# Optimization experiments

Hardware: AMD Instinct MI355X
Metric: run time of the kernel (lower is better)

The kernel has to match this reference:

```python
import jax, jax.numpy as jnp
import numpy as np

N, E, B = 10000, 160000, 64
ND, ED, H, L, C = 128, 64, 256, 4, 10
LN_EPS = 1e-5


def _layernorm(x, g, b):
    mu = jnp.mean(x, axis=-1, keepdims=True)
    var = jnp.mean(jnp.square(x - mu), axis=-1, keepdims=True)
    return (x - mu) * jax.lax.rsqrt(var + LN_EPS) * g + b


def setup_inputs() -> dict:
    key = jax.random.key(0)
    ks = jax.random.split(key, 24)

    def w(k, shape, fan_in):
        return jax.random.normal(k, shape, jnp.float32) * (1.0 / np.sqrt(fan_in))

    node_features = jax.random.normal(ks[0], (N, ND), jnp.float32)
    edge_index = jax.random.randint(ks[1], (2, E), 0, N, jnp.int64)
    edge_features = jax.random.normal(ks[2], (E, ED), jnp.float32)
    # deterministic sorted batch assignment (no empty graphs)
    batch = (jnp.arange(N, dtype=jnp.int64) * B) // N

    inp = dict(
        node_features=node_features,
        edge_index=edge_index,
        edge_features=edge_features,
        batch=batch,
        node_W=w(ks[3], (ND, H), ND), node_b=jnp.zeros((H,), jnp.float32),
        edge_W=w(ks[4], (ED, H), ED), edge_b=jnp.zeros((H,), jnp.float32),
        msg_W1=w(ks[5], (L, 3 * H, H), 3 * H), msg_b1=jnp.zeros((L, H), jnp.float32),
        msg_W2=w(ks[6], (L, H, H), H), msg_b2=jnp.zeros((L, H), jnp.float32),
        upd_W1=w(ks[7], (L, 2 * H, H), 2 * H), upd_b1=jnp.zeros((L, H), jnp.float32),
        upd_W2=w(ks[8], (L, H, H), H), upd_b2=jnp.zeros((L, H), jnp.float32),
        ln_g=jnp.ones((L, H), jnp.float32), ln_b=jnp.zeros((L, H), jnp.float32),
        ro_W1=w(ks[9], (H, H), H), ro_b1=jnp.zeros((H,), jnp.float32),
        ro_W2=w(ks[10], (H, C), H), ro_b2=jnp.zeros((C,), jnp.float32),
    )
    return inp


def _forward(node_features, edge_features, node_W, node_b, edge_W, edge_b,
             msg_W1, msg_b1, msg_W2, msg_b2, upd_W1, upd_b1, upd_W2, upd_b2,
             ln_g, ln_b, ro_W1, ro_b1, ro_W2, ro_b2, edge_index, batch):
    src, dst = edge_index[0], edge_index[1]
    x = node_features @ node_W + node_b            # [N, H]
    edge_attr = edge_features @ edge_W + edge_b    # [E, H]
    for l in range(L):
        # batched gather-MLP over all edges (vectorized version of the per-edge loop)
        m_in = jnp.concatenate([x[src], x[dst], edge_attr], axis=-1)  # [E, 3H]
        msg = jax.nn.relu(m_in @ msg_W1[l] + msg_b1[l]) @ msg_W2[l] + msg_b2[l]
        agg = jnp.zeros_like(x).at[dst].add(msg)    # scatter-add by destination
        u_in = jnp.concatenate([x, agg], axis=-1)   # [N, 2H]
        upd = jax.nn.relu(u_in @ upd_W1[l] + upd_b1[l]) @ upd_W2[l] + upd_b2[l]
        x = _layernorm(x + upd, ln_g[l], ln_b[l])
    # global mean pool per graph
    sums = jax.ops.segment_sum(x, batch, num_segments=B)
    cnts = jax.ops.segment_sum(jnp.ones((x.shape[0], 1), x.dtype), batch, num_segments=B)
    pooled = sums / cnts                            # [B, H]
    return jax.nn.relu(pooled @ ro_W1 + ro_b1) @ ro_W2 + ro_b2  # [B, C]


def reference(node_features, edge_index, edge_features, batch,
              node_W, node_b, edge_W, edge_b,
              msg_W1, msg_b1, msg_W2, msg_b2,
              upd_W1, upd_b1, upd_W2, upd_b2,
              ln_g, ln_b, ro_W1, ro_b1, ro_W2, ro_b2):
    return _forward(node_features, edge_features, node_W, node_b, edge_W, edge_b,
                    msg_W1, msg_b1, msg_W2, msg_b2, upd_W1, upd_b1, upd_W2, upd_b2,
                    ln_g, ln_b, ro_W1, ro_b1, ro_W2, ro_b2, edge_index, batch)
```

## Files before the change

### kernel.cpp

```cpp
#include <hip/hip_runtime.h>
#include <cstdint>
#include <cstddef>


typedef unsigned short u16;
typedef __attribute__((ext_vector_type(4))) float f32x4;
typedef __attribute__((ext_vector_type(8))) short bf16x8;
typedef __attribute__((ext_vector_type(4))) short s16x4;

constexpr int kN  = 10000;
constexpr int kE  = 160000;
constexpr int kB  = 64;
constexpr int kH  = 256;
constexpr int kL  = 4;
constexpr int kC  = 10;
constexpr float kEps = 1e-5f;

struct __align__(16) F4 { float v[4]; };
__device__ __forceinline__ F4 ldF4(const float* p) { return *reinterpret_cast<const F4*>(p); }

__device__ __forceinline__ u16 f2bf(float f) {
    unsigned u = __builtin_bit_cast(unsigned, f);
    return (u16)((u + 0x7fffu + ((u >> 16) & 1u)) >> 16);
}
__device__ __forceinline__ float bf2f(u16 h) {
    return __builtin_bit_cast(float, (unsigned)h << 16);
}
__device__ __forceinline__ unsigned cvtpk(float lo, float hi) {
    unsigned r;
    asm("v_cvt_pk_bf16_f32 %0, %1, %2" : "=v"(r) : "v"(lo), "v"(hi));
    return r;
}

typedef __attribute__((address_space(1))) void GV;
typedef __attribute__((address_space(3))) void LV;
__device__ __forceinline__ void gl_lds16(const void* g, void* l) {
    __builtin_amdgcn_global_load_lds((GV*)g, (LV*)l, 16, 0, 0);
}
__device__ __forceinline__ void dma_w16k(const u16* __restrict__ Wc, char* lds, int tid) {
    const int w = tid >> 6, lane = tid & 63;
    char* lb = lds + w * 4096;
    const char* gb = (const char*)Wc + w * 4096 + lane * 16;
    #pragma unroll
    for (int i = 0; i < 4; ++i) gl_lds16(gb + i * 1024, lb + i * 1024);
}

__device__ __forceinline__ bf16x8 g_frag(const u16* __restrict__ g, int n, int kg) {
    return *reinterpret_cast<const bf16x8*>(g + n * 32 + ((kg ^ ((n >> 1) & 3)) << 3));
}
__device__ __forceinline__ bf16x8 rdfrag(const char* lds, int n, int kg) {
    return *reinterpret_cast<const bf16x8*>(lds + n * 64 + ((kg ^ ((n >> 1) & 3)) << 4));
}
__device__ __forceinline__ bf16x8 rdH(const char* H, int row, int kbyte) {
    return *reinterpret_cast<const bf16x8*>(H + row * 512 + (kbyte ^ ((row & 7) << 4)));
}

__global__ void k_detect_i64(const unsigned* __restrict__ w, int* __restrict__ flag) {
    if (threadIdx.x == 0 && blockIdx.x == 0) {
        int is64 = 1;
        for (int i = 0; i < 64; ++i)
            if (w[2*i + 1] != 0u) { is64 = 0; break; }
        *flag = is64;
    }
}
__global__ void k_cvt_idx(const unsigned* __restrict__ w, const int* __restrict__ flag,
                          int* __restrict__ out, int n) {
    int i = blockIdx.x * 256 + threadIdx.x;
    if (i < n) out[i] = (*flag) ? (int)w[2*i] : (int)w[i];
}

__global__ __launch_bounds__(256) void k_hist(const int* __restrict__ dst,
                                              int* __restrict__ cnt) {
    int e = blockIdx.x * 256 + threadIdx.x;
    if (e < kE) atomicAdd(&cnt[dst[e]], 1);
}
__global__ __launch_bounds__(256) void k_scan(const int* __restrict__ cnt,
                                              int* __restrict__ cur) {
    __shared__ int part[256];
    const int t = threadIdx.x;
    const int per = (kN + 255) / 256;
    int s = 0;
    for (int i = 0; i < per; ++i) {
        int idx = t * per + i;
        if (idx < kN) s += cnt[idx];
    }
    int own = s;
    part[t] = s; __syncthreads();
    for (int off = 1; off < 256; off <<= 1) {
        int v = (t >= off) ? part[t - off] : 0;
        __syncthreads();
        part[t] += v;
        __syncthreads();
    }
    int run = part[t] - own;
    for (int i = 0; i < per; ++i) {
        int idx = t * per + i;
        if (idx < kN) { cur[idx] = run; run += cnt[idx]; }
    }
}
__global__ __launch_bounds__(256) void k_scatter(
    const int* __restrict__ src, const int* __restrict__ dst,
    int* __restrict__ cur, int* __restrict__ rank,
    int* __restrict__ ssorted, int* __restrict__ dsorted) {
    int e = blockIdx.x * 256 + threadIdx.x;
    if (e < kE) {
        int d = dst[e];
        int p = atomicAdd(&cur[d], 1);
        rank[e] = p;
        ssorted[p] = src[e];
        dsorted[p] = d;
    }
}

__global__ __launch_bounds__(256) void k_prep_w(
    const float* __restrict__ mW1, const float* __restrict__ mW2,
    const float* __restrict__ uW1, const float* __restrict__ uW2,
    u16* __restrict__ tm1, u16* __restrict__ tm2,
    u16* __restrict__ tu1, u16* __restrict__ tu2)
{
    int idx = blockIdx.x * 256 + threadIdx.x;
    const int S1 = kL * 768 * 256;
    const int S2 = S1 + kL * 256 * 256;
    const int S3 = S2 + kL * 512 * 256;
    const int S4 = S3 + kL * 256 * 256;
    const float* src; u16* dst; int K, r;
    if (idx < S1)      { src = mW1; dst = tm1; K = 768; r = idx; }
    else if (idx < S2) { src = mW2; dst = tm2; K = 256; r = idx - S1; }
    else if (idx < S3) { src = uW1; dst = tu1; K = 512; r = idx - S2; }
    else if (idx < S4) { src = uW2; dst = tu2; K = 256; r = idx - S3; }
    else return;
    int per = K * 256;
    int layer = r / per, rr = r - layer * per;
    int k = rr >> 8, n = rr & 255;
    int kc = k >> 5, kg = (k >> 3) & 3, e = k & 7;
    dst[(size_t)layer * per + (size_t)kc * 8192 + n * 32 + ((kg ^ ((n >> 1) & 3)) << 3) + e]
        = f2bf(src[(size_t)layer * per + rr]);
}

__global__ __launch_bounds__(256) void k_prep_ef(
    const float* __restrict__ ef, const int* __restrict__ rank,
    u16* __restrict__ efs)
{
    int idx = blockIdx.x * 256 + threadIdx.x;
    if (idx >= kE * 64) return;
    int e = idx >> 6, k = idx & 63;
    float v = ef[idx];
    int p = rank[e];
    int row = p & 63, blk = p >> 6;
    int kc = k >> 5, kg = (k >> 3) & 3, ee = k & 7;
    efs[(size_t)blk * 4096 + kc * 2048 + row * 32
        + ((kg ^ ((row >> 1) & 3)) << 3) + ee] = f2bf(v);
}

__global__ __launch_bounds__(256) void k_prep_m(
    const float* __restrict__ eW, const float* __restrict__ eb,
    const float* __restrict__ mW1, const float* __restrict__ mb1,
    u16* __restrict__ tmc, float* __restrict__ b1p)
{
    __shared__ float sWe[16 * 256];
    const int l = blockIdx.x, rq = blockIdx.y, t = threadIdx.x;
    const int r0 = rq * 16;
    #pragma unroll
    for (int i = 0; i < 16; ++i) sWe[i * 256 + t] = eW[(size_t)(r0 + i) * 256 + t];
    __syncthreads();
    const float* W1c = mW1 + (size_t)l * 768 * 256 + (size_t)512 * 256;
    float m[16];
    #pragma unroll
    for (int r = 0; r < 16; ++r) m[r] = 0.f;
    float bp = (rq == 0) ? mb1[l * 256 + t] : 0.f;
    for (int j = 0; j < 256; ++j) {
        float wv = W1c[(size_t)j * 256 + t];
        if (rq == 0) bp = fmaf(eb[j], wv, bp);
        #pragma unroll
        for (int r = 0; r < 16; ++r) m[r] = fmaf(sWe[r * 256 + j], wv, m[r]);
    }
    if (rq == 0) b1p[l * 256 + t] = bp;
    #pragma unroll
    for (int r = 0; r < 16; ++r) {
        int k = r0 + r;
        int kc = k >> 5, kg = (k >> 3) & 3, e = k & 7;
        tmc[(size_t)l * 16384 + (size_t)kc * 8192 + t * 32
            + ((kg ^ ((t >> 1) & 3)) << 3) + e] = f2bf(m[r]);
    }
}

__global__ __launch_bounds__(256) void k_encode_nodes(
    const float* __restrict__ nf, const float* __restrict__ W,
    const float* __restrict__ b, float* __restrict__ x, u16* __restrict__ x_bf)
{
    __shared__ float s_nf[4 * 128];
    const int n0 = blockIdx.x * 4;
    const int tid = threadIdx.x;
    reinterpret_cast<float2*>(s_nf)[tid] =
        reinterpret_cast<const float2*>(nf + (size_t)n0 * 128)[tid];
    __syncthreads();
    float acc[4] = {0.f, 0.f, 0.f, 0.f};
    for (int k = 0; k < 128; ++k) {
        float w = W[k * kH + tid];
        #pragma unroll
        for (int r = 0; r < 4; ++r) acc[r] = fmaf(s_nf[r * 128 + k], w, acc[r]);
    }
    float bias = b[tid];
    #pragma unroll
    for (int r = 0; r < 4; ++r) {
        float o = acc[r] + bias;
        x[(size_t)(n0 + r) * kH + tid] = o;
        x_bf[(size_t)(n0 + r) * kH + tid] = f2bf(o);
    }
}

__global__ __launch_bounds__(256, 3) void k_node_pre(
    const u16* __restrict__ x_bf, const u16* __restrict__ Wt1,
    u16* __restrict__ y_a, u16* __restrict__ y_b)
{
    __shared__ char sWt[16384];
    __shared__ char sA[4096];
    const int tid = threadIdx.x;
    const int n0 = blockIdx.x * 64;
    const int half = blockIdx.y;
    const u16* Wt = Wt1 + (size_t)half * 8 * 8192;
    u16* y = half ? y_b : y_a;
    const int w = tid >> 6, lane = tid & 63;
    const int lr = lane & 15, lg = lane >> 4;
    const int srow = tid >> 2, skg = tid & 3;
    const int kg_src = skg ^ ((srow >> 1) & 3);
    int gnode = n0 + srow; if (gnode >= kN) gnode = kN - 1;

    f32x4 acc[4][4];
    #pragma unroll
    for (int i = 0; i < 4; ++i)
        #pragma unroll
        for (int j = 0; j < 4; ++j) acc[i][j] = (f32x4){0.f, 0.f, 0.f, 0.f};

    for (int kc = 0; kc < 8; ++kc) {
        __syncthreads();
        dma_w16k(Wt + (size_t)kc * 8192, sWt, tid);
        gl_lds16(x_bf + (size_t)gnode * kH + kc * 32 + kg_src * 8, sA + w * 1024);
        __syncthreads();
        bf16x8 af[4], bfm[4];
        #pragma unroll
        for (int i = 0; i < 4; ++i) af[i] = rdfrag(sWt, w * 64 + i * 16 + lr, lg);
        #pragma unroll
        for (int j = 0; j < 4; ++j) bfm[j] = rdfrag(sA, j * 16 + lr, lg);
        #pragma unroll
        for (int i = 0; i < 4; ++i)
            #pragma unroll
            for (int j = 0; j < 4; ++j)
                acc[i][j] = __builtin_amdgcn_mfma_f32_16x16x32_bf16(af[i], bfm[j], acc[i][j], 0, 0, 0);
    }
    #pragma unroll
    for (int i = 0; i < 4; ++i) {
        const int hc0 = w * 64 + i * 16 + lg * 4;
        #pragma unroll
        for (int j = 0; j < 4; ++j) {
            const int node = n0 + j * 16 + lr;
            if (node < kN) {
                uint2 o;
                o.x = cvtpk(acc[i][j][0], acc[i][j][1]);
                o.y = cvtpk(acc[i][j][2], acc[i][j][3]);
                *reinterpret_cast<uint2*>(y + (size_t)node * kH + hc0) = o;
            }
        }
    }
}

__global__ __launch_bounds__(256, 4) void k_msg(
    const u16* __restrict__ efs,
    const int* __restrict__ ssorted, const int* __restrict__ dsorted,
    const u16* __restrict__ y_a, const u16* __restrict__ y_b,
    const u16* __restrict__ Wtm, const float* __restrict__ b1p,
    const u16* __restrict__ Wt2, const float* __restrict__ b2,
    float* __restrict__ agg)
{
    __shared__ char sH[32768];
    __shared__ int sDst[64];

    const int tid = threadIdx.x;
    const int nwg = gridDim.x;
    const int q8 = nwg >> 3, r8 = nwg & 7;
    const int xcd = blockIdx.x & 7, sub = blockIdx.x >> 3;
    const int bid = (xcd < r8 ? xcd * (q8 + 1) : r8 * (q8 + 1) + (xcd - r8) * q8) + sub;
    const int e0 = bid * 64;

    const int w = tid >> 6, lane = tid & 63;
    const int lr = lane & 15, lg = lane >> 4;

    if (tid < 64) sDst[tid] = dsorted[e0 + tid];

    uint2 ya[4][4], yb[4][4];
    #pragma unroll
    for (int j = 0; j < 4; ++j) {
        const int es = ssorted[e0 + j * 16 + lr];
        const int ed = dsorted[e0 + j * 16 + lr];
        const u16* pa = y_a + (size_t)es * kH;
        const u16* pb = y_b + (size_t)ed * kH;
        #pragma unroll
        for (int i = 0; i < 4; ++i) {
            const int hc0 = w * 64 + i * 16 + lg * 4;
            ya[j][i] = *reinterpret_cast<const uint2*>(pa + hc0);
            yb[j][i] = *reinterpret_cast<const uint2*>(pb + hc0);
        }
    }

    f32x4 acc[4][4];
    #pragma unroll
    for (int i = 0; i < 4; ++i)
        #pragma unroll
        for (int j = 0; j < 4; ++j) acc[i][j] = (f32x4){0.f, 0.f, 0.f, 0.f};

    #pragma unroll
    for (int kc = 0; kc < 2; ++kc) {
        const u16* efc = efs + (size_t)bid * 4096 + kc * 2048;
        bf16x8 af[4], bfm[4];
        #pragma unroll
        for (int i = 0; i < 4; ++i) af[i] = g_frag(Wtm + kc * 8192, w * 64 + i * 16 + lr, lg);
        #pragma unroll
        for (int j = 0; j < 4; ++j) {
            int row = j * 16 + lr;
            bfm[j] = *reinterpret_cast<const bf16x8*>(
                efc + row * 32 + ((lg ^ ((row >> 1) & 3)) << 3));
        }
        #pragma unroll
        for (int i = 0; i < 4; ++i)
            #pragma unroll
            for (int j = 0; j < 4; ++j)
                acc[i][j] = __builtin_amdgcn_mfma_f32_16x16x32_bf16(af[i], bfm[j], acc[i][j], 0, 0, 0);
    }

    #pragma unroll
    for (int j = 0; j < 4; ++j) {
        const int edge = j * 16 + lr;
        #pragma unroll
        for (int i = 0; i < 4; ++i) {
            const int hc0 = w * 64 + i * 16 + lg * 4;
            const F4 bb = ldF4(b1p + hc0);
            float s0 = __builtin_bit_cast(float, ya[j][i].x << 16) + __builtin_bit_cast(float, yb[j][i].x << 16);
            float s1 = __builtin_bit_cast(float, ya[j][i].x & 0xffff0000u) + __builtin_bit_cast(float, yb[j][i].x & 0xffff0000u);
            float s2 = __builtin_bit_cast(float, ya[j][i].y << 16) + __builtin_bit_cast(float, yb[j][i].y << 16);
            float s3 = __builtin_bit_cast(float, ya[j][i].y & 0xffff0000u) + __builtin_bit_cast(float, yb[j][i].y & 0xffff0000u);
            float h0 = acc[i][j][0] + bb.v[0] + s0; h0 = h0 > 0.f ? h0 : 0.f;
            float h1 = acc[i][j][1] + bb.v[1] + s1; h1 = h1 > 0.f ? h1 : 0.f;
            float h2 = acc[i][j][2] + bb.v[2] + s2; h2 = h2 > 0.f ? h2 : 0.f;
            float h3 = acc[i][j][3] + bb.v[3] + s3; h3 = h3 > 0.f ? h3 : 0.f;
            uint2 o; o.x = cvtpk(h0, h1); o.y = cvtpk(h2, h3);
            int byte = edge * 512 + hc0 * 2;
            *reinterpret_cast<uint2*>(sH + (byte ^ ((edge & 7) << 4))) = o;
            acc[i][j] = (f32x4){0.f, 0.f, 0.f, 0.f};
        }
    }
    __syncthreads();

    #pragma unroll 2
    for (int kc = 0; kc < 8; ++kc) {
        bf16x8 af2[4], bf2[4];
        #pragma unroll
        for (int i = 0; i < 4; ++i) af2[i] = rdH(sH, i * 16 + lr, kc * 64 + lg * 16);
        #pragma unroll
        for (int j = 0; j < 4; ++j) bf2[j] = g_frag(Wt2 + kc * 8192, w * 64 + j * 16 + lr, lg);
        #pragma unroll
        for (int i = 0; i < 4; ++i)
            #pragma unroll
            for (int j = 0; j < 4; ++j)
                acc[i][j] = __builtin_amdgcn_mfma_f32_16x16x32_bf16(af2[i], bf2[j], acc[i][j], 0, 0, 0);
    }

    __syncthreads();
    #pragma unroll
    for (int j = 0; j < 4; ++j) {
        const int oc = w * 64 + j * 16 + lr;
        const float b2v = b2[oc];
        #pragma unroll
        for (int i = 0; i < 4; ++i) {
            unsigned p01 = cvtpk(acc[i][j][0] + b2v, acc[i][j][1] + b2v);
            unsigned p23 = cvtpk(acc[i][j][2] + b2v, acc[i][j][3] + b2v);
            int eb0 = i * 16 + lg * 4;
            *reinterpret_cast<u16*>(sH + (((eb0 + 0) * 512 + oc * 2) ^ (((eb0 + 0) & 7) << 4))) = (u16)p01;
            *reinterpret_cast<u16*>(sH + (((eb0 + 1) * 512 + oc * 2) ^ (((eb0 + 1) & 7) << 4))) = (u16)(p01 >> 16);
            *reinterpret_cast<u16*>(sH + (((eb0 + 2) * 512 + oc * 2) ^ (((eb0 + 2) & 7) << 4))) = (u16)p23;
            *reinterpret_cast<u16*>(sH + (((eb0 + 3) * 512 + oc * 2) ^ (((eb0 + 3) & 7) << 4))) = (u16)(p23 >> 16);
        }
    }
    __syncthreads();

    {
        const int col = tid;
        float run = 0.f;
        int prev = sDst[0];
        #pragma unroll 1
        for (int eb = 0; eb < 8; ++eb) {
            float vv[8]; int dd[8];
            #pragma unroll
            for (int t = 0; t < 8; ++t) {
                int e = eb * 8 + t;
                int byte = e * 512 + col * 2;
                vv[t] = bf2f(*reinterpret_cast<const u16*>(sH + (byte ^ ((e & 7) << 4))));
                dd[t] = sDst[e];
            }
            #pragma unroll
            for (int t = 0; t < 8; ++t) {
                if (dd[t] != prev) {
                    unsafeAtomicAdd(agg + (size_t)prev * kH + col, run);
                    run = 0.f; prev = dd[t];
                }
                run += vv[t];
            }
        }
        unsafeAtomicAdd(agg + (size_t)prev * kH + col, run);
    }
}

__global__ __launch_bounds__(256, 2) void k_upd(
    float* __restrict__ x, u16* __restrict__ x_bf,
    float* __restrict__ agg,
    const u16* __restrict__ Wt1, const float* __restrict__ b1,
    const u16* __restrict__ Wt2, const float* __restrict__ b2,
    const float* __restrict__ lng, const float* __restrict__ lnb)
{
    __shared__ char sWt[2][16384];
    __shared__ char sA[2][4096];
    __shared__ char sH[32768];

    const int tid = threadIdx.x;
    const int n0 = blockIdx.x * 64;
    const int w = tid >> 6, lane = tid & 63;
    const int lr = lane & 15, lg = lane >> 4;
    const int srow = tid >> 2, skg = tid & 3;
    const int kg_src = skg ^ ((srow >> 1) & 3);
    int gnode = n0 + srow; if (gnode >= kN) gnode = kN - 1;

    dma_w16k(Wt1, sWt[0], tid);
    gl_lds16(x_bf + (size_t)gnode * kH + kg_src * 8, sA[0] + w * 1024);

    f32x4 acc[4][4];
    #pragma unroll
    for (int i = 0; i < 4; ++i)
        #pragma unroll
        for (int j = 0; j < 4; ++j) acc[i][j] = (f32x4){0.f, 0.f, 0.f, 0.f};
    __syncthreads();

    for (int kc = 0; kc < 16; ++kc) {
        const int cur = kc & 1, nxt = cur ^ 1;
        bool do_agg = false; F4 a0, a1;
        if (kc < 15) {
            dma_w16k(Wt1 + (size_t)(kc + 1) * 8192, sWt[nxt], tid);
            if (kc + 1 < 8) {
                gl_lds16(x_bf + (size_t)gnode * kH + (kc + 1) * 32 + kg_src * 8,
                         sA[nxt] + w * 1024);
            } else {
                const float* ap = agg + (size_t)gnode * kH + (kc + 1 - 8) * 32 + skg * 8;
                a0 = ldF4(ap); a1 = ldF4(ap + 4); do_agg = true;
            }
        } else {
            dma_w16k(Wt2, sWt[nxt], tid);
        }
        bf16x8 af[4], bfm[4];
        #pragma unroll
        for (int i = 0; i < 4; ++i) af[i] = rdfrag(sWt[cur], w * 64 + i * 16 + lr, lg);
        #pragma unroll
        for (int j = 0; j < 4; ++j) bfm[j] = rdfrag(sA[cur], j * 16 + lr, lg);
        #pragma unroll
        for (int i = 0; i < 4; ++i)
            #pragma unroll
            for (int j = 0; j < 4; ++j)
                acc[i][j] = __builtin_amdgcn_mfma_f32_16x16x32_bf16(af[i], bfm[j], acc[i][j], 0, 0, 0);
        if (do_agg) {
            int4 bv;
            bv.x = (int)cvtpk(a0.v[0], a0.v[1]);
            bv.y = (int)cvtpk(a0.v[2], a0.v[3]);
            bv.z = (int)cvtpk(a1.v[0], a1.v[1]);
            bv.w = (int)cvtpk(a1.v[2], a1.v[3]);
            *reinterpret_cast<int4*>(sA[nxt] + srow * 64 + ((skg ^ ((srow >> 1) & 3)) << 4)) = bv;
        }
        __syncthreads();
    }

    #pragma unroll
    for (int i = 0; i < 4; ++i) {
        const int hc0 = w * 64 + i * 16 + lg * 4;
        const F4 bb = ldF4(b1 + hc0);
        #pragma unroll
        for (int j = 0; j < 4; ++j) {
            const int row = j * 16 + lr;
            float h0 = acc[i][j][0] + bb.v[0]; h0 = h0 > 0.f ? h0 : 0.f;
            float h1 = acc[i][j][1] + bb.v[1]; h1 = h1 > 0.f ? h1 : 0.f;
            float h2 = acc[i][j][2] + bb.v[2]; h2 = h2 > 0.f ? h2 : 0.f;
            float h3 = acc[i][j][3] + bb.v[3]; h3 = h3 > 0.f ? h3 : 0.f;
            uint2 o; o.x = cvtpk(h0, h1); o.y = cvtpk(h2, h3);
            int byte = row * 512 + hc0 * 2;
            *reinterpret_cast<uint2*>(sH + (byte ^ ((row & 7) << 4))) = o;
            acc[i][j] = (f32x4){0.f, 0.f, 0.f, 0.f};
        }
    }
    __syncthreads();

    {
        float4 z = make_float4(0.f, 0.f, 0.f, 0.f);
        float4* bp = reinterpret_cast<float4*>(agg + (size_t)n0 * kH);
        #pragma unroll
        for (int i = 0; i < 16; ++i) {
            int idx = i * 256 + tid;
            int row = idx >> 6;
            if (n0 + row < kN) bp[idx] = z;
        }
    }

    for (int kc = 0; kc < 8; ++kc) {
        const int cur = kc & 1, nxt = cur ^ 1;
        if (kc < 7) dma_w16k(Wt2 + (size_t)(kc + 1) * 8192, sWt[nxt], tid);
        bf16x8 af2[4], bf2[4];
        #pragma unroll
        for (int i = 0; i < 4; ++i) af2[i] = rdH(sH, i * 16 + lr, kc * 64 + lg * 16);
        #pragma unroll
        for (int j = 0; j < 4; ++j) bf2[j] = rdfrag(sWt[cur], w * 64 + j * 16 + lr, lg);
        #pragma unroll
        for (int i = 0; i < 4; ++i)
            #pragma unroll
            for (int j = 0; j < 4; ++j)
                acc[i][j] = __builtin_amdgcn_mfma_f32_16x16x32_bf16(af2[i], bf2[j], acc[i][j], 0, 0, 0);
        __syncthreads();
    }

    float b2v[4], gv[4], bvn[4];
    #pragma unroll
    for (int j = 0; j < 4; ++j) {
        int oc = w * 64 + j * 16 + lr;
        b2v[j] = b2[oc]; gv[j] = lng[oc]; bvn[j] = lnb[oc];
    }
    #pragma unroll
    for (int i = 0; i < 4; ++i)
        #pragma unroll
        for (int j = 0; j < 4; ++j) {
            int oc = w * 64 + j * 16 + lr;
            #pragma unroll
            for (int q = 0; q < 4; ++q) {
                int node = n0 + i * 16 + lg * 4 + q;
                int ncl = node < kN ? node : kN - 1;
                acc[i][j][q] += b2v[j] + x[(size_t)ncl * kH + oc];
            }
        }

    float (*red)[64][2] = reinterpret_cast<float(*)[64][2]>(sA[0]);
    float2* mstd = reinterpret_cast<float2*>(sA[0] + 2048);
    __syncthreads();
    #pragma unroll
    for (int i = 0; i < 4; ++i)
        #pragma unroll
        for (int q = 0; q < 4; ++q) {
            float s = acc[i][0][q] + acc[i][1][q] + acc[i][2][q] + acc[i][3][q];
            float ss = acc[i][0][q] * acc[i][0][q] + acc[i][1][q] * acc[i][1][q]
                     + acc[i][2][q] * acc[i][2][q] + acc[i][3][q] * acc[i][3][q];
            #pragma unroll
            for (int m = 1; m < 16; m <<= 1) { s += __shfl_xor(s, m); ss += __shfl_xor(ss, m); }
            if (lr == 0) { red[w][i * 16 + lg * 4 + q][0] = s; red[w][i * 16 + lg * 4 + q][1] = ss; }
        }
    __syncthreads();
    if (tid < 64) {
        float s = red[0][tid][0] + red[1][tid][0] + red[2][tid][0] + red[3][tid][0];
        float ss = red[0][tid][1] + red[1][tid][1] + red[2][tid][1] + red[3][tid][1];
        float mean = s * (1.f / 256.f);
        float var = ss * (1.f / 256.f) - mean * mean;
        mstd[tid] = make_float2(mean, rsqrtf(var + kEps));
    }
    __syncthreads();
    #pragma unroll
    for (int i = 0; i < 4; ++i)
        #pragma unroll
        for (int j = 0; j < 4; ++j) {
            int oc = w * 64 + j * 16 + lr;
            #pragma unroll
            for (int q = 0; q < 4; ++q) {
                int nn = i * 16 + lg * 4 + q;
                int node = n0 + nn;
                if (node < kN) {
                    float2 ms = mstd[nn];
                    float o = (acc[i][j][q] - ms.x) * ms.y * gv[j] + bvn[j];
                    x[(size_t)node * kH + oc] = o;
                    x_bf[(size_t)node * kH + oc] = f2bf(o);
                }
            }
        }
}

__device__ __forceinline__ int lower_bound_i(const int* a, int n, int v) {
    int lo = 0, hi = n;
    while (lo < hi) { int m = (lo + hi) >> 1; if (a[m] < v) lo = m + 1; else hi = m; }
    return lo;
}

__global__ __launch_bounds__(256) void k_pool_ro(
    const float* __restrict__ x, const int* __restrict__ batch,
    const float* __restrict__ W1, const float* __restrict__ b1,
    const float* __restrict__ W2, const float* __restrict__ b2,
    float* __restrict__ out)
{
    __shared__ float ph[kH];
    __shared__ float h1[kH];
    const int b = blockIdx.x, t = threadIdx.x;
    const int s = lower_bound_i(batch, kN, b);
    const int e = lower_bound_i(batch, kN, b + 1);
    float acc = 0.f;
    for (int i = s; i < e; ++i) acc += x[(size_t)i * kH + t];
    ph[t] = acc / (float)(e - s);
    __syncthreads();
    float a = b1[t];
    for (int k = 0; k < kH; ++k) a = fmaf(ph[k], W1[k * kH + t], a);
    h1[t] = a > 0.f ? a : 0.f;
    __syncthreads();
    if (t < kC) {
        float o = b2[t];
        for (int k = 0; k < kH; ++k) o = fmaf(h1[k], W2[k * kC + t], o);
        out[b * kC + t] = o;
    }
}

extern "C" void kernel_launch(void* const* d_in, const int* in_sizes, int n_in,
                              void* d_out, int out_size, void* d_ws, size_t ws_size,
                              hipStream_t stream)
{
    const float* nf     = (const float*)d_in[0];
    const void*  ei_raw = d_in[1];
    const float* ef     = (const float*)d_in[2];
    const void*  ba_raw = d_in[3];
    const float* node_W = (const float*)d_in[4];
    const float* node_b = (const float*)d_in[5];
    const float* edge_W = (const float*)d_in[6];
    const float* edge_b = (const float*)d_in[7];
    const float* msg_W1 = (const float*)d_in[8];
    const float* msg_b1 = (const float*)d_in[9];
    const float* msg_W2 = (const float*)d_in[10];
    const float* msg_b2 = (const float*)d_in[11];
    const float* upd_W1 = (const float*)d_in[12];
    const float* upd_b1 = (const float*)d_in[13];
    const float* upd_W2 = (const float*)d_in[14];
    const float* upd_b2 = (const float*)d_in[15];
    const float* ln_g   = (const float*)d_in[16];
    const float* ln_b   = (const float*)d_in[17];
    const float* ro_W1  = (const float*)d_in[18];
    const float* ro_b1  = (const float*)d_in[19];
    const float* ro_W2  = (const float*)d_in[20];
    const float* ro_b2  = (const float*)d_in[21];

    char* p = (char*)d_ws;
    auto alloc = [&](size_t bytes) { char* r = p; p += (bytes + 255) & ~(size_t)255; return r; };
    float* x    = (float*)alloc((size_t)kN * kH * 4);
    float* agg  = (float*)alloc((size_t)kN * kH * 4);
    u16* x_bf   = (u16*)alloc((size_t)kN * kH * 2);
    u16* y_a    = (u16*)alloc((size_t)kN * kH * 2);
    u16* y_b    = (u16*)alloc((size_t)kN * kH * 2);
    u16* efs    = (u16*)alloc((size_t)kE * 64 * 2);
    u16* tm1 = (u16*)alloc((size_t)kL * 768 * 256 * 2);
    u16* tm2 = (u16*)alloc((size_t)kL * 256 * 256 * 2);
    u16* tu1 = (u16*)alloc((size_t)kL * 512 * 256 * 2);
    u16* tu2 = (u16*)alloc((size_t)kL * 256 * 256 * 2);
    u16* tmc = (u16*)alloc((size_t)kL * 64 * 256 * 2);
    float* b1p = (float*)alloc((size_t)kL * 256 * 4);
    int* ei32 = (int*)alloc((size_t)2 * kE * 4);
    int* ba32 = (int*)alloc((size_t)kN * 4);
    int* cnt  = (int*)alloc((size_t)kN * 4);
    int* cur  = (int*)alloc((size_t)kN * 4);
    int* rank = (int*)alloc((size_t)kE * 4);
    int* ssorted = (int*)alloc((size_t)kE * 4);
    int* dsorted = (int*)alloc((size_t)kE * 4);
    int* flag = (int*)alloc(4);

    k_detect_i64<<<1, 64, 0, stream>>>((const unsigned*)ei_raw, flag);
    k_cvt_idx<<<(2 * kE + 255) / 256, 256, 0, stream>>>((const unsigned*)ei_raw, flag, ei32, 2 * kE);
    k_cvt_idx<<<(kN + 255) / 256, 256, 0, stream>>>((const unsigned*)ba_raw, flag, ba32, kN);
    const int* src = ei32;
    const int* dst = ei32 + kE;

    hipMemsetAsync(cnt, 0, (size_t)kN * 4, stream);
    k_hist<<<(kE + 255) / 256, 256, 0, stream>>>(dst, cnt);
    k_scan<<<1, 256, 0, stream>>>(cnt, cur);
    k_scatter<<<(kE + 255) / 256, 256, 0, stream>>>(src, dst, cur, rank, ssorted, dsorted);

    const int prep_elems = kL * (768 + 256 + 512 + 256) * 256;
    k_prep_w<<<(prep_elems + 255) / 256, 256, 0, stream>>>(
        msg_W1, msg_W2, upd_W1, upd_W2, tm1, tm2, tu1, tu2);
    k_prep_m<<<dim3(kL, 4), 256, 0, stream>>>(edge_W, edge_b, msg_W1, msg_b1, tmc, b1p);
    k_prep_ef<<<(kE * 64 + 255) / 256, 256, 0, stream>>>(ef, rank, efs);

    k_encode_nodes<<<kN / 4, 256, 0, stream>>>(nf, node_W, node_b, x, x_bf);
    hipMemsetAsync(agg, 0, (size_t)kN * kH * sizeof(float), stream);

    for (int l = 0; l < kL; ++l) {
        k_node_pre<<<dim3((kN + 63) / 64, 2), 256, 0, stream>>>(
            x_bf, tm1 + (size_t)l * 768 * 256, y_a, y_b);
        k_msg<<<kE / 64, 256, 0, stream>>>(efs, ssorted, dsorted, y_a, y_b,
            tmc + (size_t)l * 64 * 256, b1p + l * 256,
            tm2 + (size_t)l * 256 * 256, msg_b2 + l * kH, agg);
        k_upd<<<(kN + 63) / 64, 256, 0, stream>>>(x, x_bf, agg,
            tu1 + (size_t)l * 512 * 256, upd_b1 + l * kH,
            tu2 + (size_t)l * 256 * 256, upd_b2 + l * kH,
            ln_g + l * kH, ln_b + l * kH);
    }

    k_pool_ro<<<kB, 256, 0, stream>>>(x, ba32, ro_W1, ro_b1, ro_W2, ro_b2, (float*)d_out);
}
```

Measured before the change: 607.0 us.

## Move x-half of update GEMM into node_pre, shrink upd tiles, split pooling

The x-dependent half of the update MLP's first layer is now computed in k_node_pre as a third output (y_c), so k_upd only multiplies the aggregated messages and adds y_c before the ReLU. k_upd tiles 32 nodes per block instead of 64 and raises its occupancy bound, giving more blocks and less LDS per block. Pooling is split across four partial blocks per graph with atomic accumulation, followed by a separate readout kernel. The cost is an extra bf16 intermediate round trip, extra precision loss from storing y_c in bf16, and an additional kernel launch.

New measurement: 555.8 us. -8.4%, faster.

```diff
diff --git a/kernel.cpp b/kernel.cpp
--- a/kernel.cpp
+++ b/kernel.cpp
@@ -210,16 +210,17 @@
 }
 
 __global__ __launch_bounds__(256, 3) void k_node_pre(
-    const u16* __restrict__ x_bf, const u16* __restrict__ Wt1,
-    u16* __restrict__ y_a, u16* __restrict__ y_b)
+    const u16* __restrict__ x_bf, const u16* __restrict__ Wtm1,
+    const u16* __restrict__ Wtu1,
+    u16* __restrict__ y_a, u16* __restrict__ y_b, u16* __restrict__ y_c)
 {
     __shared__ char sWt[16384];
     __shared__ char sA[4096];
     const int tid = threadIdx.x;
     const int n0 = blockIdx.x * 64;
     const int half = blockIdx.y;
-    const u16* Wt = Wt1 + (size_t)half * 8 * 8192;
-    u16* y = half ? y_b : y_a;
+    const u16* Wt = (half == 2) ? Wtu1 : Wtm1 + (size_t)half * 8 * 8192;
+    u16* y = (half == 0) ? y_a : (half == 1 ? y_b : y_c);
     const int w = tid >> 6, lane = tid & 63;
     const int lr = lane & 15, lg = lane >> 4;
     const int srow = tid >> 2, skg = tid & 3;
@@ -409,61 +410,68 @@
     }
 }
 
-__global__ __launch_bounds__(256, 2) void k_upd(
+__global__ __launch_bounds__(256, 3) void k_upd(
     float* __restrict__ x, u16* __restrict__ x_bf,
     float* __restrict__ agg,
-    const u16* __restrict__ Wt1, const float* __restrict__ b1,
+    const u16* __restrict__ Wt1b, const float* __restrict__ b1,
     const u16* __restrict__ Wt2, const float* __restrict__ b2,
-    const float* __restrict__ lng, const float* __restrict__ lnb)
+    const float* __restrict__ lng, const float* __restrict__ lnb,
+    const u16* __restrict__ y_c)
 {
     __shared__ char sWt[2][16384];
-    __shared__ char sA[2][4096];
-    __shared__ char sH[32768];
+    __shared__ char sA[2][2048];
+    __shared__ char sH[16384];
 
     const int tid = threadIdx.x;
-    const int n0 = blockIdx.x * 64;
+    const int n0 = blockIdx.x * 32;
     const int w = tid >> 6, lane = tid & 63;
     const int lr = lane & 15, lg = lane >> 4;
     const int srow = tid >> 2, skg = tid & 3;
-    const int kg_src = skg ^ ((srow >> 1) & 3);
-    int gnode = n0 + srow; if (gnode >= kN) gnode = kN - 1;
-
-    dma_w16k(Wt1, sWt[0], tid);
-    gl_lds16(x_bf + (size_t)gnode * kH + kg_src * 8, sA[0] + w * 1024);
+    int gnode = n0 + (srow & 31); if (gnode >= kN) gnode = kN - 1;
+    const bool stg = tid < 128;
 
     f32x4 acc[4][4];
     #pragma unroll
     for (int i = 0; i < 4; ++i)
         #pragma unroll
         for (int j = 0; j < 4; ++j) acc[i][j] = (f32x4){0.f, 0.f, 0.f, 0.f};
-    __syncthreads();
-
-    for (int kc = 0; kc < 16; ++kc) {
+
+    dma_w16k(Wt1b, sWt[0], tid);
+    if (stg) {
+        const float* ap = agg + (size_t)gnode * kH + skg * 8;
+        F4 a0 = ldF4(ap), a1 = ldF4(ap + 4);
+        int4 bv;
+        bv.x = (int)cvtpk(a0.v[0], a0.v[1]);
+        bv.y = (int)cvtpk(a0.v[2], a0.v[3]);
+        bv.z = (int)cvtpk(a1.v[0], a1.v[1]);
+        bv.w = (int)cvtpk(a1.v[2], a1.v[3]);
+        *reinterpret_cast<int4*>(sA[0] + srow * 64 + ((skg ^ ((srow >> 1) & 3)) << 4)) = bv;
+    }
+    __syncthreads();
+
+    for (int kc = 0; kc < 8; ++kc) {
         const int cur = kc & 1, nxt = cur ^ 1;
-        bool do_agg = false; F4 a0, a1;
-        if (kc < 15) {
-            dma_w16k(Wt1 + (size_t)(kc + 1) * 8192, sWt[nxt], tid);
-            if (kc + 1 < 8) {
-                gl_lds16(x_bf + (size_t)gnode * kH + (kc + 1) * 32 + kg_src * 8,
-                         sA[nxt] + w * 1024);
-            } else {
-                const float* ap = agg + (size_t)gnode * kH + (kc + 1 - 8) * 32 + skg * 8;
-                a0 = ldF4(ap); a1 = ldF4(ap + 4); do_agg = true;
+        bool pf = false; F4 a0, a1;
+        if (kc < 7) {
+            dma_w16k(Wt1b + (size_t)(kc + 1) * 8192, sWt[nxt], tid);
+            if (stg) {
+                const float* ap = agg + (size_t)gnode * kH + (kc + 1) * 32 + skg * 8;
+                a0 = ldF4(ap); a1 = ldF4(ap + 4); pf = true;
             }
         } else {
             dma_w16k(Wt2, sWt[nxt], tid);
         }
-        bf16x8 af[4], bfm[4];
+        bf16x8 af[4], bfm[2];
         #pragma unroll
         for (int i = 0; i < 4; ++i) af[i] = rdfrag(sWt[cur], w * 64 + i * 16 + lr, lg);
         #pragma unroll
-        for (int j = 0; j < 4; ++j) bfm[j] = rdfrag(sA[cur], j * 16 + lr, lg);
+        for (int j = 0; j < 2; ++j) bfm[j] = rdfrag(sA[cur], j * 16 + lr, lg);
         #pragma unroll
         for (int i = 0; i < 4; ++i)
             #pragma unroll
-            for (int j = 0; j < 4; ++j)
+            for (int j = 0; j < 2; ++j)
                 acc[i][j] = __builtin_amdgcn_mfma_f32_16x16x32_bf16(af[i], bfm[j], acc[i][j], 0, 0, 0);
-        if (do_agg) {
+        if (pf) {
             int4 bv;
             bv.x = (int)cvtpk(a0.v[0], a0.v[1]);
             bv.y = (int)cvtpk(a0.v[2], a0.v[3]);
@@ -479,12 +487,18 @@
         const int hc0 = w * 64 + i * 16 + lg * 4;
         const F4 bb = ldF4(b1 + hc0);
         #pragma unroll
-        for (int j = 0; j < 4; ++j) {
+        for (int j = 0; j < 2; ++j) {
             const int row = j * 16 + lr;
-            float h0 = acc[i][j][0] + bb.v[0]; h0 = h0 > 0.f ? h0 : 0.f;
-            float h1 = acc[i][j][1] + bb.v[1]; h1 = h1 > 0.f ? h1 : 0.f;
-            float h2 = acc[i][j][2] + bb.v[2]; h2 = h2 > 0.f ? h2 : 0.f;
-            float h3 = acc[i][j][3] + bb.v[3]; h3 = h3 > 0.f ? h3 : 0.f;
+            int ncl = n0 + row; if (ncl >= kN) ncl = kN - 1;
+            uint2 yc = *reinterpret_cast<const uint2*>(y_c + (size_t)ncl * kH + hc0);
+            float s0 = __builtin_bit_cast(float, yc.x << 16);
+            float s1 = __builtin_bit_cast(float, yc.x & 0xffff0000u);
+            float s2 = __builtin_bit_cast(float, yc.y << 16);
+            float s3 = __builtin_bit_cast(float, yc.y & 0xffff0000u);
+            float h0 = acc[i][j][0] + bb.v[0] + s0; h0 = h0 > 0.f ? h0 : 0.f;
+            float h1 = acc[i][j][1] + bb.v[1] + s1; h1 = h1 > 0.f ? h1 : 0.f;
+            float h2 = acc[i][j][2] + bb.v[2] + s2; h2 = h2 > 0.f ? h2 : 0.f;
+            float h3 = acc[i][j][3] + bb.v[3] + s3; h3 = h3 > 0.f ? h3 : 0.f;
             uint2 o; o.x = cvtpk(h0, h1); o.y = cvtpk(h2, h3);
             int byte = row * 512 + hc0 * 2;
             *reinterpret_cast<uint2*>(sH + (byte ^ ((row & 7) << 4))) = o;
@@ -497,7 +511,7 @@
         float4 z = make_float4(0.f, 0.f, 0.f, 0.f);
         float4* bp = reinterpret_cast<float4*>(agg + (size_t)n0 * kH);
         #pragma unroll
-        for (int i = 0; i < 16; ++i) {
+        for (int i = 0; i < 8; ++i) {
             int idx = i * 256 + tid;
             int row = idx >> 6;
             if (n0 + row < kN) bp[idx] = z;
@@ -507,13 +521,13 @@
     for (int kc = 0; kc < 8; ++kc) {
         const int cur = kc & 1, nxt = cur ^ 1;
         if (kc < 7) dma_w16k(Wt2 + (size_t)(kc + 1) * 8192, sWt[nxt], tid);
-        bf16x8 af2[4], bf2[4];
-        #pragma unroll
-        for (int i = 0; i < 4; ++i) af2[i] = rdH(sH, i * 16 + lr, kc * 64 + lg * 16);
+        bf16x8 af2[2], bf2[4];
+        #pragma unroll
+        for (int i = 0; i < 2; ++i) af2[i] = rdH(sH, i * 16 + lr, kc * 64 + lg * 16);
         #pragma unroll
         for (int j = 0; j < 4; ++j) bf2[j] = rdfrag(sWt[cur], w * 64 + j * 16 + lr, lg);
         #pragma unroll
-        for (int i = 0; i < 4; ++i)
+        for (int i = 0; i < 2; ++i)
             #pragma unroll
             for (int j = 0; j < 4; ++j)
                 acc[i][j] = __builtin_amdgcn_mfma_f32_16x16x32_bf16(af2[i], bf2[j], acc[i][j], 0, 0, 0);
@@ -527,7 +541,7 @@
         b2v[j] = b2[oc]; gv[j] = lng[oc]; bvn[j] = lnb[oc];
     }
     #pragma unroll
-    for (int i = 0; i < 4; ++i)
+    for (int i = 0; i < 2; ++i)
         #pragma unroll
         for (int j = 0; j < 4; ++j) {
             int oc = w * 64 + j * 16 + lr;
@@ -539,11 +553,10 @@
             }
         }
 
-    float (*red)[64][2] = reinterpret_cast<float(*)[64][2]>(sA[0]);
-    float2* mstd = reinterpret_cast<float2*>(sA[0] + 2048);
-    __syncthreads();
-    #pragma unroll
-    for (int i = 0; i < 4; ++i)
+    float (*red)[32][2] = reinterpret_cast<float(*)[32][2]>(sA[0]);
+    float2* mstd = reinterpret_cast<float2*>((char*)sA[0] + 1024);
+    #pragma unroll
+    for (int i = 0; i < 2; ++i)
         #pragma unroll
         for (int q = 0; q < 4; ++q) {
             float s = acc[i][0][q] + acc[i][1][q] + acc[i][2][q] + acc[i][3][q];
@@ -554,7 +567,7 @@
             if (lr == 0) { red[w][i * 16 + lg * 4 + q][0] = s; red[w][i * 16 + lg * 4 + q][1] = ss; }
         }
     __syncthreads();
-    if (tid < 64) {
+    if (tid < 32) {
         float s = red[0][tid][0] + red[1][tid][0] + red[2][tid][0] + red[3][tid][0];
         float ss = red[0][tid][1] + red[1][tid][1] + red[2][tid][1] + red[3][tid][1];
         float mean = s * (1.f / 256.f);
@@ -563,7 +576,7 @@
     }
     __syncthreads();
     #pragma unroll
-    for (int i = 0; i < 4; ++i)
+    for (int i = 0; i < 2; ++i)
         #pragma unroll
         for (int j = 0; j < 4; ++j) {
             int oc = w * 64 + j * 16 + lr;
@@ -587,8 +600,23 @@
     return lo;
 }
 
-__global__ __launch_bounds__(256) void k_pool_ro(
+__global__ __launch_bounds__(256) void k_pool_part(
     const float* __restrict__ x, const int* __restrict__ batch,
+    float* __restrict__ pooled)
+{
+    const int b = blockIdx.x >> 2, q = blockIdx.x & 3, t = threadIdx.x;
+    const int s = lower_bound_i(batch, kN, b);
+    const int e = lower_bound_i(batch, kN, b + 1);
+    const int len = e - s;
+    const int qs = s + (len * q) / 4;
+    const int qe = s + (len * (q + 1)) / 4;
+    float acc = 0.f;
+    for (int i = qs; i < qe; ++i) acc += x[(size_t)i * kH + t];
+    unsafeAtomicAdd(pooled + b * kH + t, acc);
+}
+
+__global__ __launch_bounds__(256) void k_ro(
+    const float* __restrict__ pooled, const int* __restrict__ batch,
     const float* __restrict__ W1, const float* __restrict__ b1,
     const float* __restrict__ W2, const float* __restrict__ b2,
     float* __restrict__ out)
@@ -598,9 +626,7 @@
     const int b = blockIdx.x, t = threadIdx.x;
     const int s = lower_bound_i(batch, kN, b);
     const int e = lower_bound_i(batch, kN, b + 1);
-    float acc = 0.f;
-    for (int i = s; i < e; ++i) acc += x[(size_t)i * kH + t];
-    ph[t] = acc / (float)(e - s);
+    ph[t] = pooled[b * kH + t] / (float)(e - s);
     __syncthreads();
     float a = b1[t];
     for (int k = 0; k < kH; ++k) a = fmaf(ph[k], W1[k * kH + t], a);
@@ -644,9 +670,11 @@
     auto alloc = [&](size_t bytes) { char* r = p; p += (bytes + 255) & ~(size_t)255; return r; };
     float* x    = (float*)alloc((size_t)kN * kH * 4);
     float* agg  = (float*)alloc((size_t)kN * kH * 4);
+    float* pooled = (float*)alloc((size_t)kB * kH * 4);
     u16* x_bf   = (u16*)alloc((size_t)kN * kH * 2);
     u16* y_a    = (u16*)alloc((size_t)kN * kH * 2);
     u16* y_b    = (u16*)alloc((size_t)kN * kH * 2);
+    u16* y_c    = (u16*)alloc((size_t)kN * kH * 2);
     u16* efs    = (u16*)alloc((size_t)kE * 64 * 2);
     u16* tm1 = (u16*)alloc((size_t)kL * 768 * 256 * 2);
     u16* tm2 = (u16*)alloc((size_t)kL * 256 * 256 * 2);
@@ -682,18 +710,21 @@
 
     k_encode_nodes<<<kN / 4, 256, 0, stream>>>(nf, node_W, node_b, x, x_bf);
     hipMemsetAsync(agg, 0, (size_t)kN * kH * sizeof(float), stream);
+    hipMemsetAsync(pooled, 0, (size_t)kB * kH * sizeof(float), stream);
 
     for (int l = 0; l < kL; ++l) {
-        k_node_pre<<<dim3((kN + 63) / 64, 2), 256, 0, stream>>>(
-            x_bf, tm1 + (size_t)l * 768 * 256, y_a, y_b);
+        k_node_pre<<<dim3((kN + 63) / 64, 3), 256, 0, stream>>>(
+            x_bf, tm1 + (size_t)l * 768 * 256, tu1 + (size_t)l * 512 * 256,
+            y_a, y_b, y_c);
         k_msg<<<kE / 64, 256, 0, stream>>>(efs, ssorted, dsorted, y_a, y_b,
             tmc + (size_t)l * 64 * 256, b1p + l * 256,
             tm2 + (size_t)l * 256 * 256, msg_b2 + l * kH, agg);
-        k_upd<<<(kN + 63) / 64, 256, 0, stream>>>(x, x_bf, agg,
-            tu1 + (size_t)l * 512 * 256, upd_b1 + l * kH,
+        k_upd<<<(kN + 31) / 32, 256, 0, stream>>>(x, x_bf, agg,
+            tu1 + (size_t)l * 512 * 256 + 8 * 8192, upd_b1 + l * kH,
             tu2 + (size_t)l * 256 * 256, upd_b2 + l * kH,
-            ln_g + l * kH, ln_b + l * kH);
-    }
-
-    k_pool_ro<<<kB, 256, 0, stream>>>(x, ba32, ro_W1, ro_b1, ro_W2, ro_b2, (float*)d_out);
-}
+            ln_g + l * kH, ln_b + l * kH, y_c);
+    }
+
+    k_pool_part<<<kB * 4, 256, 0, stream>>>(x, ba32, pooled);
+    k_ro<<<kB, 256, 0, stream>>>(pooled, ba32, ro_W1, ro_b1, ro_W2, ro_b2, (float*)d_out);
+}
```
